# Kernel optimization log

Measured on AMD Instinct MI355X. Metric: run time of the kernel, lower is better.

The kernel has to match this reference:

```python
import jax, jax.numpy as jnp
import numpy as np

POOL = 3      # pooling_size
EPS = 0.006   # constant added to each segment mean in the original code


def setup_inputs() -> dict:
    key = jax.random.key(0)
    k1, k2 = jax.random.split(key)
    B, N, D = 8, 3072, 1024          # N divisible by POOL -> no remainder branch
    steps = N // POOL
    x = jax.random.normal(k1, (B, N, D), dtype=jnp.float32)
    # (start, end) shot boundaries, sorted so start <= end, values in [0, N)
    graph = jnp.sort(jax.random.randint(k2, (B, steps, 2), 0, N, dtype=jnp.int64), axis=-1)
    return {"x": x, "graph": graph}


def reference(x, graph):
    B, N, D = x.shape
    steps = N // POOL
    # Exclusive+inclusive prefix sums: c[b, k] = sum over x[b, :k]  -> [B, N+1, D]
    c = jnp.concatenate([jnp.zeros((B, 1, D), x.dtype), jnp.cumsum(x, axis=1)], axis=1)
    s = graph[..., 0]                # [B, steps]
    e = graph[..., 1]                # [B, steps]
    idx_e = jnp.broadcast_to((e + 1)[..., None], (B, steps, D))
    idx_s = jnp.broadcast_to(s[..., None], (B, steps, D))
    seg_sum = jnp.take_along_axis(c, idx_e, axis=1) - jnp.take_along_axis(c, idx_s, axis=1)
    seg_len = (e - s + 1).astype(x.dtype)[..., None]
    seg_mean = seg_sum / seg_len + EPS            # [B, steps, D]
    # fixed-size window mean over consecutive POOL frames
    win_mean = x.reshape(B, steps, POOL, D).mean(axis=2)   # [B, steps, D]
    # original appends (segment mean, window mean) per step -> interleave
    out = jnp.stack([seg_mean, win_mean], axis=2).reshape(B, 2 * steps, D)
    return out
```

## Files before the change

### kernel.cpp

```cpp
#include <hip/hip_runtime.h>


constexpr int Bdim  = 8;
constexpr int Nn    = 3072;
constexpr int Dd    = 1024;
constexpr int STEPS = 1024;
constexpr int CHW   = 8;
constexpr int CHR   = 24;
constexpr int NCH   = 128;
constexpr int KT    = 4;
constexpr int NKT   = 256;
constexpr int D4    = Dd / 4;
constexpr int RCAP  = 12;
constexpr float EPS = 0.006f;

constexpr size_t T_E = (size_t)Bdim * 2 * STEPS * Dd;
constexpr size_t P_E = (size_t)Bdim * NCH * Dd;
constexpr size_t O_E = (size_t)Bdim * (NCH + 1) * Dd;

typedef float nat_f4 __attribute__((ext_vector_type(4)));

__device__ __forceinline__ float4 f4add(float4 a, float4 b) {
    return make_float4(a.x + b.x, a.y + b.y, a.z + b.z, a.w + b.w);
}

__device__ __forceinline__ float4 f4sel(bool c, float4 a, float4 b) {
    return make_float4(c ? a.x : b.x, c ? a.y : b.y,
                       c ? a.z : b.z, c ? a.w : b.w);
}

__device__ __forceinline__ void nt_store(float4 v, float4* p) {
    nat_f4 nv = {v.x, v.y, v.z, v.w};
    __builtin_nontemporal_store(nv, reinterpret_cast<nat_f4*>(p));
}

__device__ __forceinline__ float4 nt_load(const float4* p) {
    nat_f4 nv = __builtin_nontemporal_load(reinterpret_cast<const nat_f4*>(p));
    return make_float4(nv.x, nv.y, nv.z, nv.w);
}

__global__ __launch_bounds__(256)
void k0_bucket(const int* __restrict__ graph, int* __restrict__ rowcnt,
               int* __restrict__ evrow) {
    const int b = blockIdx.x;
    __shared__ int cnt[Nn];
    for (int i = threadIdx.x; i < Nn; i += 256) cnt[i] = 0;
    __syncthreads();
    for (int k = threadIdx.x; k < STEPS; k += 256) {
        const int2 se = *reinterpret_cast<const int2*>(
            graph + ((size_t)(b * STEPS + k)) * 2);
        const int s  = se.x;
        const int ie = se.y + 1;
        int sl = atomicAdd(&cnt[s], 1);
        if (sl < RCAP)
            evrow[((size_t)b * Nn + s) * RCAP + sl] = 2 * k;
        if (ie < Nn) {
            int sl2 = atomicAdd(&cnt[ie], 1);
            if (sl2 < RCAP)
                evrow[((size_t)b * Nn + ie) * RCAP + sl2] = 2 * k + 1;
        }
    }
    __syncthreads();
    for (int i = threadIdx.x; i < Nn; i += 256)
        rowcnt[(size_t)b * Nn + i] = min(cnt[i], RCAP);
}

__global__ __launch_bounds__(256)
void k1_scan(const float4* __restrict__ x4, float4* __restrict__ out4,
             float4* __restrict__ T4, float4* __restrict__ P4,
             const int* __restrict__ rowcnt, const int* __restrict__ evrow) {
    const int t  = threadIdx.x;
    const int ch = blockIdx.x;
    const int b  = blockIdx.y;
    const int k0 = ch * CHW;
    const int r0 = ch * CHR;
    const float4 z4 = make_float4(0.f, 0.f, 0.f, 0.f);

    const float4* xp = x4   + ((size_t)(b * Nn + r0)) * D4 + t;
    float4*       op = out4 + ((size_t)b * 2 * STEPS) * D4 + t;
    float4*       Tb = T4   + ((size_t)b * 2 * STEPS) * D4 + t;
    const int*    rc = rowcnt + (size_t)b * Nn + r0;
    const int*    ev = evrow + ((size_t)b * Nn + r0) * RCAP;

    float4 v[CHR];
#pragma unroll
    for (int i = 0; i < CHR; ++i)
        v[i] = nt_load(&xp[(size_t)i * D4]);

#pragma unroll
    for (int wi = 0; wi < CHW; ++wi) {
        float4 w = f4add(f4add(v[3 * wi], v[3 * wi + 1]), v[3 * wi + 2]);
        float4 wm = make_float4(w.x * (1.f / 3.f), w.y * (1.f / 3.f),
                                w.z * (1.f / 3.f), w.w * (1.f / 3.f));
        nt_store(wm, &op[(size_t)(2 * (k0 + wi) + 1) * D4]);
    }

    float4 run = z4;
#pragma unroll
    for (int j = 0; j < CHR; ++j) {
        const int nj = rc[j];
        for (int q = 0; q < nj; ++q) {
            const int trow = ev[j * RCAP + q];
            Tb[(size_t)trow * D4] = run;
        }
        run = f4add(run, v[j]);
    }
    P4[((size_t)b * NCH + ch) * D4 + t] = run;
}

__global__ __launch_bounds__(256)
void k2_chscan(const float4* __restrict__ P4, float4* __restrict__ O4) {
    __shared__ float4 part[8][33];
    const int cw  = threadIdx.x & 31;
    const int seg = threadIdx.x >> 5;
    const int col = blockIdx.x * 32 + cw;
    const int b   = blockIdx.y;

    const float4* p = P4 + (size_t)b * NCH * D4 + col;
    float4 v[16];
    float4 sum = make_float4(0.f, 0.f, 0.f, 0.f);
#pragma unroll
    for (int i = 0; i < 16; ++i) {
        v[i] = p[(size_t)(seg * 16 + i) * D4];
        sum = f4add(sum, v[i]);
    }
    part[seg][cw] = sum;
    __syncthreads();
    if (threadIdx.x < 32) {
        float4 run = make_float4(0.f, 0.f, 0.f, 0.f);
#pragma unroll
        for (int s = 0; s < 8; ++s) {
            float4 t2 = part[s][threadIdx.x];
            part[s][threadIdx.x] = run;
            run = f4add(run, t2);
        }
    }
    __syncthreads();
    float4 run = part[seg][cw];
    float4* o = O4 + (size_t)b * (NCH + 1) * D4 + col;
#pragma unroll
    for (int i = 0; i < 16; ++i) {
        o[(size_t)(seg * 16 + i) * D4] = run;
        run = f4add(run, v[i]);
    }
    if (seg == 7) o[(size_t)NCH * D4] = run;
}

__global__ __launch_bounds__(256)
void k4_combine(const float4* __restrict__ T4, const float4* __restrict__ O4,
                const int* __restrict__ graph, float4* __restrict__ out4) {
    const int t  = threadIdx.x;
    const int kt = blockIdx.x;
    const int b  = blockIdx.y;

    const int* gp = graph + ((size_t)(b * STEPS + kt * KT)) * 2;
    const int4 ga = *reinterpret_cast<const int4*>(gp);
    const int4 gb = *reinterpret_cast<const int4*>(gp + 4);
    const int sA[KT] = {ga.x, ga.z, gb.x, gb.z};
    const int eA[KT] = {ga.y, ga.w, gb.y, gb.w};

    const float4* Tb = T4 + (size_t)b * 2 * STEPS * D4 + t;
    const float4* oc = O4 + (size_t)b * (NCH + 1) * D4 + t;
    float4*       ob = out4 + (size_t)b * 2 * STEPS * D4 + t;

    float4 ts[KT], te[KT], o1[KT], o2[KT];
    int ieA[KT];
    const float4 tot = oc[(size_t)NCH * D4];
#pragma unroll
    for (int u = 0; u < KT; ++u) {
        const int k = kt * KT + u;
        ts[u] = Tb[(size_t)(2 * k) * D4];
        te[u] = Tb[(size_t)(2 * k + 1) * D4];
        const int s = sA[u];
        const int ie = eA[u] + 1;  ieA[u] = ie;
        o1[u] = oc[(size_t)(s / CHR) * D4];
        const int c2 = ie < Nn ? ie / CHR : 0;
        o2[u] = oc[(size_t)c2 * D4];
    }

#pragma unroll
    for (int u = 0; u < KT; ++u) {
        float4 cs = f4add(o1[u], ts[u]);
        float4 ce = f4sel(ieA[u] < Nn, f4add(o2[u], te[u]), tot);

        float inv = 1.f / (float)(eA[u] - sA[u] + 1);
        float4 res = make_float4((ce.x - cs.x) * inv + EPS,
                                 (ce.y - cs.y) * inv + EPS,
                                 (ce.z - cs.z) * inv + EPS,
                                 (ce.w - cs.w) * inv + EPS);
        const int k = kt * KT + u;
        nt_store(res, &ob[(size_t)(2 * k) * D4]);
    }
}

extern "C" void kernel_launch(void* const* d_in, const int* in_sizes, int n_in,
                              void* d_out, int out_size, void* d_ws, size_t ws_size,
                              hipStream_t stream) {
    const float* x     = (const float*)d_in[0];
    const int*   graph = (const int*)d_in[1];
    float*       out   = (float*)d_out;

    float* T = (float*)d_ws;
    float* P = T + T_E;
    float* O = P + P_E;
    int*   rowcnt = (int*)(O + O_E);
    int*   evrow  = rowcnt + (size_t)Bdim * Nn;

    k0_bucket<<<dim3(Bdim), 256, 0, stream>>>(graph, rowcnt, evrow);
    dim3 g1(NCH, Bdim);
    k1_scan<<<g1, 256, 0, stream>>>((const float4*)x, (float4*)out,
                                    (float4*)T, (float4*)P, rowcnt, evrow);
    dim3 g2(D4 / 32, Bdim);
    k2_chscan<<<g2, 256, 0, stream>>>((const float4*)P, (float4*)O);
    dim3 g4(NKT, Bdim);
    k4_combine<<<g4, 256, 0, stream>>>((const float4*)T, (const float4*)O,
                                       graph, (float4*)out);
}
```

Baseline: 193.2 us.

## Fold event bucketing into scan kernel using per-block shared-memory lists

```diff
diff --git a/kernel.cpp b/kernel.cpp
--- a/kernel.cpp
+++ b/kernel.cpp
@@ -11,12 +11,11 @@
 constexpr int KT    = 4;
 constexpr int NKT   = 256;
 constexpr int D4    = Dd / 4;
-constexpr int RCAP  = 12;
+constexpr int RCAP  = 16;
 constexpr float EPS = 0.006f;
 
 constexpr size_t T_E = (size_t)Bdim * 2 * STEPS * Dd;
 constexpr size_t P_E = (size_t)Bdim * NCH * Dd;
-constexpr size_t O_E = (size_t)Bdim * (NCH + 1) * Dd;
 
 typedef float nat_f4 __attribute__((ext_vector_type(4)));
 
@@ -40,35 +39,9 @@
 }
 
 __global__ __launch_bounds__(256)
-void k0_bucket(const int* __restrict__ graph, int* __restrict__ rowcnt,
-               int* __restrict__ evrow) {
-    const int b = blockIdx.x;
-    __shared__ int cnt[Nn];
-    for (int i = threadIdx.x; i < Nn; i += 256) cnt[i] = 0;
-    __syncthreads();
-    for (int k = threadIdx.x; k < STEPS; k += 256) {
-        const int2 se = *reinterpret_cast<const int2*>(
-            graph + ((size_t)(b * STEPS + k)) * 2);
-        const int s  = se.x;
-        const int ie = se.y + 1;
-        int sl = atomicAdd(&cnt[s], 1);
-        if (sl < RCAP)
-            evrow[((size_t)b * Nn + s) * RCAP + sl] = 2 * k;
-        if (ie < Nn) {
-            int sl2 = atomicAdd(&cnt[ie], 1);
-            if (sl2 < RCAP)
-                evrow[((size_t)b * Nn + ie) * RCAP + sl2] = 2 * k + 1;
-        }
-    }
-    __syncthreads();
-    for (int i = threadIdx.x; i < Nn; i += 256)
-        rowcnt[(size_t)b * Nn + i] = min(cnt[i], RCAP);
-}
-
-__global__ __launch_bounds__(256)
-void k1_scan(const float4* __restrict__ x4, float4* __restrict__ out4,
-             float4* __restrict__ T4, float4* __restrict__ P4,
-             const int* __restrict__ rowcnt, const int* __restrict__ evrow) {
+void k1_scan(const float4* __restrict__ x4, const int* __restrict__ graph,
+             float4* __restrict__ out4, float4* __restrict__ T4,
+             float4* __restrict__ P4) {
     const int t  = threadIdx.x;
     const int ch = blockIdx.x;
     const int b  = blockIdx.y;
@@ -76,17 +49,33 @@
     const int r0 = ch * CHR;
     const float4 z4 = make_float4(0.f, 0.f, 0.f, 0.f);
 
-    const float4* xp = x4   + ((size_t)(b * Nn + r0)) * D4 + t;
-    float4*       op = out4 + ((size_t)b * 2 * STEPS) * D4 + t;
-    float4*       Tb = T4   + ((size_t)b * 2 * STEPS) * D4 + t;
-    const int*    rc = rowcnt + (size_t)b * Nn + r0;
-    const int*    ev = evrow + ((size_t)b * Nn + r0) * RCAP;
-
+    const float4* xp = x4 + ((size_t)(b * Nn + r0)) * D4 + t;
     float4 v[CHR];
 #pragma unroll
     for (int i = 0; i < CHR; ++i)
         v[i] = nt_load(&xp[(size_t)i * D4]);
 
+    __shared__ int cnt[CHR];
+    __shared__ int lst[CHR][RCAP];
+    if (t < CHR) cnt[t] = 0;
+    __syncthreads();
+    for (int k = t; k < STEPS; k += 256) {
+        const int2 se = *reinterpret_cast<const int2*>(
+            graph + ((size_t)(b * STEPS + k)) * 2);
+        const int js = se.x - r0;
+        if (js >= 0 && js < CHR) {
+            int p = atomicAdd(&cnt[js], 1);
+            if (p < RCAP) lst[js][p] = 2 * k;
+        }
+        const int je = se.y + 1 - r0;
+        if (je >= 0 && je < CHR) {
+            int p = atomicAdd(&cnt[je], 1);
+            if (p < RCAP) lst[je][p] = 2 * k + 1;
+        }
+    }
+    __syncthreads();
+
+    float4* op = out4 + ((size_t)b * 2 * STEPS) * D4 + t;
 #pragma unroll
     for (int wi = 0; wi < CHW; ++wi) {
         float4 w = f4add(f4add(v[3 * wi], v[3 * wi + 1]), v[3 * wi + 2]);
@@ -95,14 +84,13 @@
         nt_store(wm, &op[(size_t)(2 * (k0 + wi) + 1) * D4]);
     }
 
+    float4* Tb = T4 + ((size_t)b * 2 * STEPS) * D4 + t;
     float4 run = z4;
 #pragma unroll
     for (int j = 0; j < CHR; ++j) {
-        const int nj = rc[j];
-        for (int q = 0; q < nj; ++q) {
-            const int trow = ev[j * RCAP + q];
-            Tb[(size_t)trow * D4] = run;
-        }
+        const int nj = min(cnt[j], RCAP);
+        for (int q = 0; q < nj; ++q)
+            Tb[(size_t)lst[j][q] * D4] = run;
         run = f4add(run, v[j]);
     }
     P4[((size_t)b * NCH + ch) * D4 + t] = run;
@@ -203,13 +191,10 @@
     float* T = (float*)d_ws;
     float* P = T + T_E;
     float* O = P + P_E;
-    int*   rowcnt = (int*)(O + O_E);
-    int*   evrow  = rowcnt + (size_t)Bdim * Nn;
-
-    k0_bucket<<<dim3(Bdim), 256, 0, stream>>>(graph, rowcnt, evrow);
+
     dim3 g1(NCH, Bdim);
-    k1_scan<<<g1, 256, 0, stream>>>((const float4*)x, (float4*)out,
-                                    (float4*)T, (float4*)P, rowcnt, evrow);
+    k1_scan<<<g1, 256, 0, stream>>>((const float4*)x, graph, (float4*)out,
+                                    (float4*)T, (float4*)P);
     dim3 g2(D4 / 32, Bdim);
     k2_chscan<<<g2, 256, 0, stream>>>((const float4*)P, (float4*)O);
     dim3 g4(NKT, Bdim);
```

Result: faster. 182.3 us (-5.6%).
